# Performance work log

Measured on AMD Instinct MI355X. Metric: run time of the kernel, lower is better.

Reference implementation:

```python
import jax, jax.numpy as jnp
import numpy as np

B, QS, KS, E, H = 2, 2048, 2048, 2048, 16
D = E // H  # head_dim = 128
EPS = 1e-6


def setup_inputs() -> dict:
    key = jax.random.key(0)
    ks = jax.random.split(key, 11)
    scale_in = 1.0 / np.sqrt(E)  # lecun_normal fan_in = E
    scale_out = 1.0 / np.sqrt(E)  # fan_in for out proj = H*D = E
    return {
        "q": jax.random.normal(ks[0], (B, QS, E), jnp.float32),
        "kv": jax.random.normal(ks[1], (B, KS, E), jnp.float32),
        "q_pos": jax.random.normal(ks[2], (B, QS, E), jnp.float32),
        "kv_pos": jax.random.normal(ks[3], (B, KS, E), jnp.float32),
        "mask": jax.random.bernoulli(ks[4], 0.5, (B, QS, KS)),
        "wq": jax.random.normal(ks[5], (E, H, D), jnp.float32) * scale_in,
        "wk": jax.random.normal(ks[6], (E, H, D), jnp.float32) * scale_in,
        "wv": jax.random.normal(ks[7], (E, H, D), jnp.float32) * scale_in,
        "q_ln_scale": jnp.ones((D,), jnp.float32),
        "k_ln_scale": jnp.ones((D,), jnp.float32),
        "wo": jax.random.normal(ks[8], (H, D, E), jnp.float32) * scale_out,
    }


def _layernorm_no_bias(x, scale):
    # flax LayerNorm over last axis, use_bias=False, epsilon=1e-6
    mu = jnp.mean(x, axis=-1, keepdims=True)
    var = jnp.mean(jnp.square(x - mu), axis=-1, keepdims=True)
    return (x - mu) * jax.lax.rsqrt(var + EPS) * scale


def reference(q, kv, q_pos, kv_pos, mask, wq, wk, wv, q_ln_scale, k_ln_scale, wo):
    dtype = q.dtype
    qi = q + q_pos          # [b, qs, e]
    ki = kv + kv_pos        # [b, ks, e]
    vi = kv
    # QKV projections (DenseGeneral, no bias) -> [b, s, h, d]
    qh = jnp.einsum('bqe,ehd->bqhd', qi, wq)
    kh = jnp.einsum('bke,ehd->bkhd', ki, wk)
    vh = jnp.einsum('bke,ehd->bkhd', vi, wv)
    # normalize_qk: LayerNorm (no bias) on query/key over head_dim
    qh = _layernorm_no_bias(qh, q_ln_scale)
    kh = _layernorm_no_bias(kh, k_ln_scale)
    # scaled dot-product with float32 logits
    qh = qh / jnp.sqrt(jnp.asarray(D, dtype))
    logits = jnp.einsum('bqhd,bkhd->bhqk', qh, kh,
                        preferred_element_type=jnp.float32)
    big_neg = jnp.finfo(jnp.float32).min
    logits = jnp.where(mask[:, None, :, :], logits, big_neg)
    attn = jax.nn.softmax(logits, axis=-1).astype(dtype)  # [b,h,q,k]
    out = jnp.einsum('bhqk,bkhd->bqhd', attn, vh)
    # output projection (DenseGeneral over (h,d), no bias)
    return jnp.einsum('bqhd,hde->bqe', out, wo)
```

## Files before the change

### kernel.cpp

```cpp
#include <hip/hip_runtime.h>
#include <hip/hip_bf16.h>


typedef __attribute__((ext_vector_type(8))) __bf16 bf16x8;
typedef __attribute__((ext_vector_type(4))) float f32x4;
typedef __attribute__((ext_vector_type(8))) unsigned short ushort8;
typedef __attribute__((ext_vector_type(4))) unsigned short ushort4v;
typedef __attribute__((ext_vector_type(4))) unsigned uint4v;
typedef __attribute__((ext_vector_type(4))) float float4v;

#define MFMA16(a, b, c) __builtin_amdgcn_mfma_f32_16x16x32_bf16((a), (b), (c), 0, 0, 0)

__device__ __forceinline__ unsigned short f2bf(float f) {
  unsigned u = __builtin_bit_cast(unsigned, f);
  u += 0x7fffu + ((u >> 16) & 1u);
  return (unsigned short)(u >> 16);
}

__device__ __forceinline__ unsigned pkbf(float lo, float hi) {
  unsigned d;
  asm("v_cvt_pk_bf16_f32 %0, %1, %2" : "=v"(d) : "v"(lo), "v"(hi));
  return d;
}

__device__ __forceinline__ float max3f(float a, float b, float c) {
  float d;
  asm("v_max3_f32 %0, %1, %2, %3" : "=v"(d) : "v"(a), "v"(b), "v"(c));
  return d;
}

__device__ __forceinline__ float exp2a(float x) {
  float d;
  asm("v_exp_f32 %0, %1" : "=v"(d) : "v"(x));
  return d;
}

__device__ __forceinline__ void gload_lds16(const void* g, void* l) {
  __builtin_amdgcn_global_load_lds(
      (const __attribute__((address_space(1))) void*)g,
      (__attribute__((address_space(3))) void*)l, 16, 0, 0);
}

__global__ __launch_bounds__(256) void k_cvt(const float4v* __restrict__ x,
                                             const float4v* __restrict__ y,
                                             ushort4v* __restrict__ o, int n4) {
  int i = blockIdx.x * 256 + threadIdx.x;
  if (i >= n4) return;
  float4v a = x[i];
  if (y) { float4v b = y[i]; a = a + b; }
  ushort4v r;
  r[0] = f2bf(a[0]); r[1] = f2bf(a[1]); r[2] = f2bf(a[2]); r[3] = f2bf(a[3]);
  o[i] = r;
}

__global__ __launch_bounds__(256) void k_cvt2(const float4v* __restrict__ x,
                                              const float4v* __restrict__ y,
                                              ushort4v* __restrict__ oa,
                                              ushort4v* __restrict__ ob, int n4) {
  int i = blockIdx.x * 256 + threadIdx.x;
  if (i >= n4) return;
  float4v a = x[i];
  float4v s = a + y[i];
  ushort4v ra, rb;
  ra[0] = f2bf(s[0]); ra[1] = f2bf(s[1]); ra[2] = f2bf(s[2]); ra[3] = f2bf(s[3]);
  rb[0] = f2bf(a[0]); rb[1] = f2bf(a[1]); rb[2] = f2bf(a[2]); rb[3] = f2bf(a[3]);
  oa[i] = ra; ob[i] = rb;
}

__global__ __launch_bounds__(256) void k_tr(const float* __restrict__ s0, const float* __restrict__ s1,
                                            const float* __restrict__ s2, const float* __restrict__ s3,
                                            unsigned short* __restrict__ d0, unsigned short* __restrict__ d1,
                                            unsigned short* __restrict__ d2, unsigned short* __restrict__ d3) {
  __shared__ float t[32][33];
  const float* S; unsigned short* D;
  switch (blockIdx.z) {
    case 0: S = s0; D = d0; break;
    case 1: S = s1; D = d1; break;
    case 2: S = s2; D = d2; break;
    default: S = s3; D = d3; break;
  }
  int x = threadIdx.x & 31, y = threadIdx.x >> 5;
  int r0 = blockIdx.y * 32, c0 = blockIdx.x * 32;
#pragma unroll
  for (int i = 0; i < 4; ++i) t[y + 8 * i][x] = S[(size_t)(r0 + y + 8 * i) * 2048 + c0 + x];
  __syncthreads();
#pragma unroll
  for (int i = 0; i < 4; ++i)
    D[(size_t)(c0 + y + 8 * i) * 2048 + r0 + x] = f2bf(t[x][y + 8 * i]);
}

__global__ __launch_bounds__(256) void k_mask(const int* __restrict__ m,
                                              unsigned long long* __restrict__ out) {
  int i = blockIdx.x * 256 + threadIdx.x;
  unsigned long long b = __ballot(m[i] != 0);
  if ((threadIdx.x & 63) == 0) out[i >> 6] = b;
}

__global__ __launch_bounds__(256) void k_trv(const unsigned short* __restrict__ Vh,
                                             unsigned short* __restrict__ Vt) {
  __shared__ unsigned short t[64][72];
  int bh = blockIdx.z;
  int s0 = blockIdx.x * 64, d0 = blockIdx.y * 64;
  size_t base = (size_t)bh * 2048 * 128;
  int row = threadIdx.x >> 2, c16 = (threadIdx.x & 3) * 16;
  {
    const unsigned short* src = Vh + base + (size_t)(s0 + row) * 128 + d0 + c16;
    ushort8 a0 = *(const ushort8*)src;
    ushort8 a1 = *(const ushort8*)(src + 8);
#pragma unroll
    for (int e = 0; e < 8; ++e) {
      t[c16 + e][row] = a0[e];
      t[c16 + 8 + e][row] = a1[e];
    }
  }
  __syncthreads();
  {
    unsigned short* dst = Vt + base + (size_t)(d0 + row) * 2048 + s0 + c16;
    *(ushort8*)dst = *(const ushort8*)&t[row][c16];
    *(ushort8*)(dst + 8) = *(const ushort8*)&t[row][c16 + 8];
  }
}

template <int MODE>
__global__ __launch_bounds__(256) void k_gemm(const unsigned short* __restrict__ A,
                                              const unsigned short* __restrict__ Bt,
                                              void* __restrict__ Cv,
                                              const float* __restrict__ lnsc) {
  constexpr int K = 2048;
  __shared__ __attribute__((aligned(16))) unsigned short sA[128 * 64];
  __shared__ __attribute__((aligned(16))) unsigned short sB[128 * 64];
  __shared__ float sSum[2][128];
  __shared__ float sSq[2][128];
  int tid = threadIdx.x;
  int lane = tid & 63, w = tid >> 6;
  int wr = w >> 1, wc = w & 1;
  int r15 = lane & 15, blk = lane >> 4;
  int n0 = blockIdx.x * 128, m0 = blockIdx.y * 128;
  const unsigned short* Abase = A + (size_t)m0 * K;
  const unsigned short* Bbase = Bt + (size_t)n0 * K;
  f32x4 acc[4][4] = {};

  for (int kt = 0; kt < K; kt += 64) {
#pragma unroll
    for (int i = 0; i < 4; ++i) {
      int c = i * 256 + tid;
      int row = c >> 3, cc = c & 7;
      gload_lds16(Abase + (size_t)row * K + kt + ((cc ^ (row & 7)) * 8), &sA[c * 8]);
    }
#pragma unroll
    for (int i = 0; i < 4; ++i) {
      int c = i * 256 + tid;
      int row = c >> 3, cc = c & 7;
      gload_lds16(Bbase + (size_t)row * K + kt + ((cc ^ (row & 7)) * 8), &sB[c * 8]);
    }
    __syncthreads();
#pragma unroll
    for (int kk = 0; kk < 2; ++kk) {
      bf16x8 av[4], bv[4];
#pragma unroll
      for (int i = 0; i < 4; ++i) {
        int row = wr * 64 + i * 16 + r15;
        av[i] = *(const bf16x8*)&sA[row * 64 + (((kk * 4 + blk) ^ (row & 7)) * 8)];
      }
#pragma unroll
      for (int j = 0; j < 4; ++j) {
        int row = wc * 64 + j * 16 + r15;
        bv[j] = *(const bf16x8*)&sB[row * 64 + (((kk * 4 + blk) ^ (row & 7)) * 8)];
      }
#pragma unroll
      for (int i = 0; i < 4; ++i)
#pragma unroll
        for (int j = 0; j < 4; ++j) acc[i][j] = MFMA16(av[i], bv[j], acc[i][j]);
    }
    __syncthreads();
  }

  if constexpr (MODE == 3) {
    float* C = (float*)Cv;
#pragma unroll
    for (int i = 0; i < 4; ++i)
#pragma unroll
      for (int r = 0; r < 4; ++r)
#pragma unroll
        for (int j = 0; j < 4; ++j) {
          int rowl = wr * 64 + i * 16 + blk * 4 + r;
          int coll = wc * 64 + j * 16 + r15;
          C[(size_t)(m0 + rowl) * 2048 + n0 + coll] = acc[i][j][r];
        }
    return;
  } else {
    if constexpr (MODE == 1 || MODE == 2) {
#pragma unroll
      for (int i = 0; i < 4; ++i)
#pragma unroll
        for (int r = 0; r < 4; ++r) {
          float sm = 0.f, sq = 0.f;
#pragma unroll
          for (int j = 0; j < 4; ++j) { float v = acc[i][j][r]; sm += v; sq += v * v; }
          sm += __shfl_xor(sm, 1); sq += __shfl_xor(sq, 1);
          sm += __shfl_xor(sm, 2); sq += __shfl_xor(sq, 2);
          sm += __shfl_xor(sm, 4); sq += __shfl_xor(sq, 4);
          sm += __shfl_xor(sm, 8); sq += __shfl_xor(sq, 8);
          if (r15 == 0) {
            int rowl = wr * 64 + i * 16 + blk * 4 + r;
            sSum[wc][rowl] = sm; sSq[wc][rowl] = sq;
          }
        }
      __syncthreads();
    }
    unsigned short* Hout = (unsigned short*)Cv;
    int h = blockIdx.x;
#pragma unroll
    for (int i = 0; i < 4; ++i)
#pragma unroll
      for (int r = 0; r < 4; ++r) {
        int rowl = wr * 64 + i * 16 + blk * 4 + r;
        float mean = 0.f, rstd = 1.f;
        if constexpr (MODE == 1 || MODE == 2) {
          float sm = sSum[0][rowl] + sSum[1][rowl];
          float sq = sSq[0][rowl] + sSq[1][rowl];
          mean = sm * 0.0078125f;
          float var = sq * 0.0078125f - mean * mean;
          rstd = rsqrtf(var + 1e-6f);
        }
        int rowg = m0 + rowl;
        int b = rowg >> 11, s = rowg & 2047;
        unsigned short* orow = Hout + (((size_t)b * 16 + h) * 2048 + s) * 128;
#pragma unroll
        for (int j = 0; j < 4; ++j) {
          int d = wc * 64 + j * 16 + r15;
          float v = acc[i][j][r];
          if constexpr (MODE == 1)
            v = (v - mean) * rstd * lnsc[d] * (0.08838834764831845f * 1.4426950408889634f);
          if constexpr (MODE == 2) v = (v - mean) * rstd * lnsc[d];
          orow[d] = f2bf(v);
        }
      }
  }
}

__device__ __forceinline__ void softmax_grp(const f32x4 (&st)[4], unsigned mw0, unsigned mw1,
                                            int blk, float& mv, float& ls,
                                            f32x4 (&o)[8], bf16x8& plo, bf16x8& phi) {
  unsigned mws0 = mw0 >> (blk * 8);
  unsigned mws1 = mw1 >> (blk * 8);
  float pvv[16];
#pragma unroll
  for (int t = 0; t < 16; ++t) {
    int s = t >> 2, r = t & 3;
    unsigned mws = (s & 2) ? mws1 : mws0;
    int bit = 4 * (s & 1) + r;
    pvv[t] = ((mws >> bit) & 1u) ? st[s][r] : -1e30f;
  }
  float c0 = max3f(pvv[0], pvv[1], pvv[2]);
  float c1 = max3f(pvv[3], pvv[4], pvv[5]);
  float c2 = max3f(pvv[6], pvv[7], pvv[8]);
  float c3 = max3f(pvv[9], pvv[10], pvv[11]);
  float c4 = max3f(pvv[12], pvv[13], pvv[14]);
  float cmax = fmaxf(max3f(c0, c1, c2), max3f(c3, c4, pvv[15]));
  cmax = fmaxf(cmax, __shfl_xor(cmax, 16));
  cmax = fmaxf(cmax, __shfl_xor(cmax, 32));
  if (!__all(cmax - mv <= 11.5f)) {
    float mnew = fmaxf(mv, cmax);
    float fac = exp2a(mv - mnew);
    ls *= fac;
    float fr0 = __shfl(fac, blk * 4 + 0);
    float fr1 = __shfl(fac, blk * 4 + 1);
    float fr2 = __shfl(fac, blk * 4 + 2);
    float fr3 = __shfl(fac, blk * 4 + 3);
#pragma unroll
    for (int t8 = 0; t8 < 8; ++t8) {
      o[t8][0] *= fr0; o[t8][1] *= fr1; o[t8][2] *= fr2; o[t8][3] *= fr3;
    }
    mv = mnew;
  }
#pragma unroll
  for (int t = 0; t < 16; ++t) pvv[t] = exp2a(pvv[t] - mv);
  float s0 = (pvv[0] + pvv[1]) + (pvv[2] + pvv[3]);
  float s1 = (pvv[4] + pvv[5]) + (pvv[6] + pvv[7]);
  float s2 = (pvv[8] + pvv[9]) + (pvv[10] + pvv[11]);
  float s3 = (pvv[12] + pvv[13]) + (pvv[14] + pvv[15]);
  ls += (s0 + s1) + (s2 + s3);
  uint4v w0, w1;
#pragma unroll
  for (int j = 0; j < 4; ++j) {
    w0[j] = pkbf(pvv[2 * j], pvv[2 * j + 1]);
    w1[j] = pkbf(pvv[8 + 2 * j], pvv[9 + 2 * j]);
  }
  plo = __builtin_bit_cast(bf16x8, w0);
  phi = __builtin_bit_cast(bf16x8, w1);
}

__global__ __launch_bounds__(512, 4) void k_attn(const unsigned short* __restrict__ Qh,
                                                 const unsigned short* __restrict__ Kh,
                                                 const unsigned short* __restrict__ Vt,
                                                 const unsigned* __restrict__ maskb,
                                                 unsigned short* __restrict__ O) {
  __shared__ __attribute__((aligned(16))) char smem[65536];
  int tid = threadIdx.x, w = tid >> 6;
  int lane = tid & 63;
  int r15 = lane & 15, blk = lane >> 4;
  int bh = blockIdx.y, b = bh >> 4, h = bh & 15;
  int qb = blockIdx.x * 128;
  size_t base = (size_t)bh * (2048 * 128);
  int qrow = qb + w * 16 + r15;

  bf16x8 qf[4];
  {
    const unsigned short* qp = Qh + base + (size_t)qrow * 128 + blk * 8;
#pragma unroll
    for (int kk = 0; kk < 4; ++kk) qf[kk] = *(const bf16x8*)(qp + kk * 32);
  }
  const unsigned* mrow = maskb + ((size_t)b * 2048 + qrow) * 64;

  const unsigned short* kgp[2];
  const unsigned short* vgp[2];
#pragma unroll
  for (int i = 0; i < 2; ++i) {
    int c = i * 512 + tid;
    int rr = c >> 4, cc = c & 15;
    int key = 32 * (rr >> 5) + 8 * ((rr >> 2) & 3) + 4 * ((rr >> 4) & 1) + (rr & 3);
    kgp[i] = Kh + base + (size_t)key * 128 + ((cc ^ (rr & 7)) * 8);
    int d = c >> 3, c8 = c & 7;
    vgp[i] = Vt + base + (size_t)d * 2048 + ((c8 ^ (d & 7)) * 8);
  }

  f32x4 o[8] = {};
  float mv = -1e30f, ls = 0.f;

#pragma unroll
  for (int i = 0; i < 2; ++i) {
    int c = i * 512 + tid;
    gload_lds16(kgp[i], (unsigned short*)smem + c * 8);
    gload_lds16(vgp[i], (unsigned short*)(smem + 16384) + c * 8);
  }
  __syncthreads();

  int cur = 0;
  for (int kc = 0; kc < 2048; kc += 64) {
    if (kc + 64 < 2048) {
      char* nb = smem + ((cur ^ 1) << 15);
#pragma unroll
      for (int i = 0; i < 2; ++i) {
        int c = i * 512 + tid;
        gload_lds16(kgp[i] + (size_t)(kc + 64) * 128, (unsigned short*)nb + c * 8);
        gload_lds16(vgp[i] + (kc + 64), (unsigned short*)(nb + 16384) + c * 8);
      }
    }
    const unsigned short* sK = (const unsigned short*)(smem + (cur << 15));
    const unsigned short* sV = (const unsigned short*)(smem + (cur << 15) + 16384);

    f32x4 st[4] = {};
#pragma unroll
    for (int kk = 0; kk < 4; ++kk) {
      int cc = (4 * kk + blk) ^ (r15 & 7);
#pragma unroll
      for (int s = 0; s < 4; ++s) {
        bf16x8 kf = *(const bf16x8*)&sK[(16 * s + r15) * 128 + cc * 8];
        st[s] = MFMA16(kf, qf[kk], st[s]);
      }
    }

    unsigned mw0 = mrow[kc >> 5], mw1 = mrow[(kc >> 5) + 1];
    bf16x8 pf0, pf1;
    softmax_grp(st, mw0, mw1, blk, mv, ls, o, pf0, pf1);

#pragma unroll
    for (int t8 = 0; t8 < 8; ++t8) {
      int vr = t8 * 16 + r15;
      bf16x8 v0 = *(const bf16x8*)&sV[vr * 64 + ((blk ^ (r15 & 7)) * 8)];
      bf16x8 v1 = *(const bf16x8*)&sV[vr * 64 + (((4 + blk) ^ (r15 & 7)) * 8)];
      o[t8] = MFMA16(pf0, v0, o[t8]);
      o[t8] = MFMA16(pf1, v1, o[t8]);
    }
    __syncthreads();
    cur ^= 1;
  }

  ls += __shfl_xor(ls, 16);
  ls += __shfl_xor(ls, 32);
  float inv = 1.f / ls;
  float ir0 = __shfl(inv, blk * 4 + 0), ir1 = __shfl(inv, blk * 4 + 1);
  float ir2 = __shfl(inv, blk * 4 + 2), ir3 = __shfl(inv, blk * 4 + 3);

  float* sO = (float*)smem;
  __syncthreads();
#pragma unroll
  for (int pass = 0; pass < 2; ++pass) {
    if ((w >> 2) == pass) {
      int wl = w & 3;
#pragma unroll
      for (int t8 = 0; t8 < 8; ++t8) {
        int bi = (wl * 16 + blk * 4) * 132 + t8 * 16 + r15;
        sO[bi] = o[t8][0] * ir0;
        sO[bi + 132] = o[t8][1] * ir1;
        sO[bi + 264] = o[t8][2] * ir2;
        sO[bi + 396] = o[t8][3] * ir3;
      }
    }
    __syncthreads();
    {
      int row = tid >> 3, d0 = (tid & 7) * 16;
      int grow = qb + pass * 64 + row;
      unsigned short* op = O + (size_t)(b * 2048 + grow) * 2048 + h * 128 + d0;
      ushort8 pk0, pk1;
#pragma unroll
      for (int e = 0; e < 8; ++e) {
        pk0[e] = f2bf(sO[row * 132 + d0 + e]);
        pk1[e] = f2bf(sO[row * 132 + d0 + 8 + e]);
      }
      *(ushort8*)op = pk0;
      *(ushort8*)(op + 8) = pk1;
    }
    __syncthreads();
  }
}

extern "C" void kernel_launch(void* const* d_in, const int* in_sizes, int n_in,
                              void* d_out, int out_size, void* d_ws, size_t ws_size,
                              hipStream_t stream) {
  const float* q      = (const float*)d_in[0];
  const float* kv     = (const float*)d_in[1];
  const float* q_pos  = (const float*)d_in[2];
  const float* kv_pos = (const float*)d_in[3];
  const int*   mask   = (const int*)d_in[4];
  const float* wq     = (const float*)d_in[5];
  const float* wk     = (const float*)d_in[6];
  const float* wv     = (const float*)d_in[7];
  const float* qls    = (const float*)d_in[8];
  const float* kls    = (const float*)d_in[9];
  const float* wo     = (const float*)d_in[10];

  char* ws = (char*)d_ws;
  const size_t SZ_ACT = (size_t)4096 * 2048 * 2;
  const size_t SZ_W   = (size_t)2048 * 2048 * 2;
  unsigned short* a_q = (unsigned short*)(ws);
  unsigned short* a_k = (unsigned short*)(ws + SZ_ACT);
  unsigned short* a_v = (unsigned short*)(ws + 2 * SZ_ACT);
  unsigned short* Qh  = (unsigned short*)(ws + 3 * SZ_ACT);
  unsigned short* Kh  = (unsigned short*)(ws + 4 * SZ_ACT);
  unsigned short* Vh  = (unsigned short*)(ws + 5 * SZ_ACT);
  unsigned short* wqt = (unsigned short*)(ws + 6 * SZ_ACT);
  unsigned short* wkt = (unsigned short*)(ws + 6 * SZ_ACT + SZ_W);
  unsigned short* wvt = (unsigned short*)(ws + 6 * SZ_ACT + 2 * SZ_W);
  unsigned short* wot = (unsigned short*)(ws + 6 * SZ_ACT + 3 * SZ_W);
  unsigned*       mkb = (unsigned*)(ws + 6 * SZ_ACT + 4 * SZ_W);
  unsigned short* Ob  = a_q;
  unsigned short* Vtr = a_k;

  const size_t NEED = 6 * SZ_ACT + 4 * SZ_W + (size_t)2 * 2048 * 64 * 4;
  if (ws_size < NEED) return;

  k_cvt<<<8192, 256, 0, stream>>>((const float4v*)q, (const float4v*)q_pos, (ushort4v*)a_q, 2097152);
  k_cvt2<<<8192, 256, 0, stream>>>((const float4v*)kv, (const float4v*)kv_pos,
                                   (ushort4v*)a_k, (ushort4v*)a_v, 2097152);
  k_tr<<<dim3(64, 64, 4), 256, 0, stream>>>(wq, wk, wv, wo, wqt, wkt, wvt, wot);
  k_mask<<<32768, 256, 0, stream>>>(mask, (unsigned long long*)mkb);

  k_gemm<1><<<dim3(16, 32), 256, 0, stream>>>(a_q, wqt, Qh, qls);
  k_gemm<2><<<dim3(16, 32), 256, 0, stream>>>(a_k, wkt, Kh, kls);
  k_gemm<0><<<dim3(16, 32), 256, 0, stream>>>(a_v, wvt, Vh, nullptr);

  k_trv<<<dim3(32, 2, 32), 256, 0, stream>>>(Vh, Vtr);

  k_attn<<<dim3(16, 32), 512, 0, stream>>>(Qh, Kh, Vtr, mkb, Ob);

  k_gemm<3><<<dim3(16, 32), 256, 0, stream>>>(Ob, wot, d_out, nullptr);
}
```

Before: 353.3 us.

## Switch attention kernel to 32x32x16 MFMA with 4 waves per block

```diff
diff --git a/kernel.cpp b/kernel.cpp
--- a/kernel.cpp
+++ b/kernel.cpp
@@ -4,12 +4,14 @@
 
 typedef __attribute__((ext_vector_type(8))) __bf16 bf16x8;
 typedef __attribute__((ext_vector_type(4))) float f32x4;
+typedef __attribute__((ext_vector_type(16))) float f32x16;
 typedef __attribute__((ext_vector_type(8))) unsigned short ushort8;
 typedef __attribute__((ext_vector_type(4))) unsigned short ushort4v;
 typedef __attribute__((ext_vector_type(4))) unsigned uint4v;
 typedef __attribute__((ext_vector_type(4))) float float4v;
 
 #define MFMA16(a, b, c) __builtin_amdgcn_mfma_f32_16x16x32_bf16((a), (b), (c), 0, 0, 0)
+#define MFMA32(a, b, c) __builtin_amdgcn_mfma_f32_32x32x16_bf16((a), (b), (c), 0, 0, 0)
 
 __device__ __forceinline__ unsigned short f2bf(float f) {
   unsigned u = __builtin_bit_cast(unsigned, f);
@@ -115,9 +117,17 @@
   }
   __syncthreads();
   {
+    const int P0[8] = {0, 1, 2, 3, 8, 9, 10, 11};
+    const int P1[8] = {4, 5, 6, 7, 12, 13, 14, 15};
     unsigned short* dst = Vt + base + (size_t)(d0 + row) * 2048 + s0 + c16;
-    *(ushort8*)dst = *(const ushort8*)&t[row][c16];
-    *(ushort8*)(dst + 8) = *(const ushort8*)&t[row][c16 + 8];
+    ushort8 w0, w1;
+#pragma unroll
+    for (int e = 0; e < 8; ++e) {
+      w0[e] = t[row][c16 + P0[e]];
+      w1[e] = t[row][c16 + P1[e]];
+    }
+    *(ushort8*)dst = w0;
+    *(ushort8*)(dst + 8) = w1;
   }
 }
 
@@ -239,100 +249,47 @@
   }
 }
 
-__device__ __forceinline__ void softmax_grp(const f32x4 (&st)[4], unsigned mw0, unsigned mw1,
-                                            int blk, float& mv, float& ls,
-                                            f32x4 (&o)[8], bf16x8& plo, bf16x8& phi) {
-  unsigned mws0 = mw0 >> (blk * 8);
-  unsigned mws1 = mw1 >> (blk * 8);
-  float pvv[16];
-#pragma unroll
-  for (int t = 0; t < 16; ++t) {
-    int s = t >> 2, r = t & 3;
-    unsigned mws = (s & 2) ? mws1 : mws0;
-    int bit = 4 * (s & 1) + r;
-    pvv[t] = ((mws >> bit) & 1u) ? st[s][r] : -1e30f;
-  }
-  float c0 = max3f(pvv[0], pvv[1], pvv[2]);
-  float c1 = max3f(pvv[3], pvv[4], pvv[5]);
-  float c2 = max3f(pvv[6], pvv[7], pvv[8]);
-  float c3 = max3f(pvv[9], pvv[10], pvv[11]);
-  float c4 = max3f(pvv[12], pvv[13], pvv[14]);
-  float cmax = fmaxf(max3f(c0, c1, c2), max3f(c3, c4, pvv[15]));
-  cmax = fmaxf(cmax, __shfl_xor(cmax, 16));
-  cmax = fmaxf(cmax, __shfl_xor(cmax, 32));
-  if (!__all(cmax - mv <= 11.5f)) {
-    float mnew = fmaxf(mv, cmax);
-    float fac = exp2a(mv - mnew);
-    ls *= fac;
-    float fr0 = __shfl(fac, blk * 4 + 0);
-    float fr1 = __shfl(fac, blk * 4 + 1);
-    float fr2 = __shfl(fac, blk * 4 + 2);
-    float fr3 = __shfl(fac, blk * 4 + 3);
-#pragma unroll
-    for (int t8 = 0; t8 < 8; ++t8) {
-      o[t8][0] *= fr0; o[t8][1] *= fr1; o[t8][2] *= fr2; o[t8][3] *= fr3;
-    }
-    mv = mnew;
-  }
-#pragma unroll
-  for (int t = 0; t < 16; ++t) pvv[t] = exp2a(pvv[t] - mv);
-  float s0 = (pvv[0] + pvv[1]) + (pvv[2] + pvv[3]);
-  float s1 = (pvv[4] + pvv[5]) + (pvv[6] + pvv[7]);
-  float s2 = (pvv[8] + pvv[9]) + (pvv[10] + pvv[11]);
-  float s3 = (pvv[12] + pvv[13]) + (pvv[14] + pvv[15]);
-  ls += (s0 + s1) + (s2 + s3);
-  uint4v w0, w1;
-#pragma unroll
-  for (int j = 0; j < 4; ++j) {
-    w0[j] = pkbf(pvv[2 * j], pvv[2 * j + 1]);
-    w1[j] = pkbf(pvv[8 + 2 * j], pvv[9 + 2 * j]);
-  }
-  plo = __builtin_bit_cast(bf16x8, w0);
-  phi = __builtin_bit_cast(bf16x8, w1);
-}
-
-__global__ __launch_bounds__(512, 4) void k_attn(const unsigned short* __restrict__ Qh,
+__global__ __launch_bounds__(256, 2) void k_attn(const unsigned short* __restrict__ Qh,
                                                  const unsigned short* __restrict__ Kh,
-                                                 const unsigned short* __restrict__ Vt,
+                                                 const unsigned short* __restrict__ Vtp,
                                                  const unsigned* __restrict__ maskb,
                                                  unsigned short* __restrict__ O) {
   __shared__ __attribute__((aligned(16))) char smem[65536];
   int tid = threadIdx.x, w = tid >> 6;
   int lane = tid & 63;
-  int r15 = lane & 15, blk = lane >> 4;
+  int q31 = lane & 31, hi = lane >> 5;
   int bh = blockIdx.y, b = bh >> 4, h = bh & 15;
   int qb = blockIdx.x * 128;
   size_t base = (size_t)bh * (2048 * 128);
-  int qrow = qb + w * 16 + r15;
-
-  bf16x8 qf[4];
+  int qrow = qb + w * 32 + q31;
+
+  bf16x8 qf[8];
   {
-    const unsigned short* qp = Qh + base + (size_t)qrow * 128 + blk * 8;
-#pragma unroll
-    for (int kk = 0; kk < 4; ++kk) qf[kk] = *(const bf16x8*)(qp + kk * 32);
+    const unsigned short* qp = Qh + base + (size_t)qrow * 128 + hi * 8;
+#pragma unroll
+    for (int wd = 0; wd < 8; ++wd) qf[wd] = *(const bf16x8*)(qp + wd * 16);
   }
   const unsigned* mrow = maskb + ((size_t)b * 2048 + qrow) * 64;
 
-  const unsigned short* kgp[2];
-  const unsigned short* vgp[2];
-#pragma unroll
-  for (int i = 0; i < 2; ++i) {
-    int c = i * 512 + tid;
+  const unsigned short* kgp[4];
+  const unsigned short* vgp[4];
+#pragma unroll
+  for (int i = 0; i < 4; ++i) {
+    int c = i * 256 + tid;
     int rr = c >> 4, cc = c & 15;
-    int key = 32 * (rr >> 5) + 8 * ((rr >> 2) & 3) + 4 * ((rr >> 4) & 1) + (rr & 3);
-    kgp[i] = Kh + base + (size_t)key * 128 + ((cc ^ (rr & 7)) * 8);
+    kgp[i] = Kh + base + (size_t)rr * 128 + ((cc ^ (rr & 15)) * 8);
     int d = c >> 3, c8 = c & 7;
-    vgp[i] = Vt + base + (size_t)d * 2048 + ((c8 ^ (d & 7)) * 8);
-  }
-
-  f32x4 o[8] = {};
+    vgp[i] = Vtp + base + (size_t)d * 2048 + ((c8 ^ (d & 7)) * 8);
+  }
+
+  f32x16 o[4] = {};
   float mv = -1e30f, ls = 0.f;
 
 #pragma unroll
-  for (int i = 0; i < 2; ++i) {
-    int c = i * 512 + tid;
-    gload_lds16(kgp[i], (unsigned short*)smem + c * 8);
-    gload_lds16(vgp[i], (unsigned short*)(smem + 16384) + c * 8);
+  for (int i = 0; i < 4; ++i) {
+    int c = i * 256 + tid;
+    gload_lds16(kgp[i], smem + c * 16);
+    gload_lds16(vgp[i], smem + 16384 + c * 16);
   }
   __syncthreads();
 
@@ -341,78 +298,134 @@
     if (kc + 64 < 2048) {
       char* nb = smem + ((cur ^ 1) << 15);
 #pragma unroll
-      for (int i = 0; i < 2; ++i) {
-        int c = i * 512 + tid;
-        gload_lds16(kgp[i] + (size_t)(kc + 64) * 128, (unsigned short*)nb + c * 8);
-        gload_lds16(vgp[i] + (kc + 64), (unsigned short*)(nb + 16384) + c * 8);
+      for (int i = 0; i < 4; ++i) {
+        int c = i * 256 + tid;
+        gload_lds16(kgp[i] + (size_t)(kc + 64) * 128, nb + c * 16);
+        gload_lds16(vgp[i] + (kc + 64), nb + 16384 + c * 16);
       }
     }
     const unsigned short* sK = (const unsigned short*)(smem + (cur << 15));
     const unsigned short* sV = (const unsigned short*)(smem + (cur << 15) + 16384);
 
-    f32x4 st[4] = {};
-#pragma unroll
-    for (int kk = 0; kk < 4; ++kk) {
-      int cc = (4 * kk + blk) ^ (r15 & 7);
-#pragma unroll
-      for (int s = 0; s < 4; ++s) {
-        bf16x8 kf = *(const bf16x8*)&sK[(16 * s + r15) * 128 + cc * 8];
-        st[s] = MFMA16(kf, qf[kk], st[s]);
-      }
-    }
-
-    unsigned mw0 = mrow[kc >> 5], mw1 = mrow[(kc >> 5) + 1];
-    bf16x8 pf0, pf1;
-    softmax_grp(st, mw0, mw1, blk, mv, ls, o, pf0, pf1);
-
-#pragma unroll
-    for (int t8 = 0; t8 < 8; ++t8) {
-      int vr = t8 * 16 + r15;
-      bf16x8 v0 = *(const bf16x8*)&sV[vr * 64 + ((blk ^ (r15 & 7)) * 8)];
-      bf16x8 v1 = *(const bf16x8*)&sV[vr * 64 + (((4 + blk) ^ (r15 & 7)) * 8)];
-      o[t8] = MFMA16(pf0, v0, o[t8]);
-      o[t8] = MFMA16(pf1, v1, o[t8]);
+    unsigned mw0 = mrow[kc >> 5] >> (4 * hi);
+    unsigned mw1 = mrow[(kc >> 5) + 1] >> (4 * hi);
+
+    f32x16 st0 = {}, st1 = {};
+#pragma unroll
+    for (int wd = 0; wd < 8; ++wd) {
+      int ck = ((2 * wd + hi) ^ (q31 & 15)) * 8;
+      bf16x8 k0 = *(const bf16x8*)&sK[q31 * 128 + ck];
+      bf16x8 k1 = *(const bf16x8*)&sK[(32 + q31) * 128 + ck];
+      st0 = MFMA32(k0, qf[wd], st0);
+      st1 = MFMA32(k1, qf[wd], st1);
+    }
+
+    float pvv[32];
+#pragma unroll
+    for (int r = 0; r < 16; ++r) {
+      int bit = (r & 3) + 8 * (r >> 2);
+      pvv[r] = ((mw0 >> bit) & 1u) ? st0[r] : -1e30f;
+      pvv[16 + r] = ((mw1 >> bit) & 1u) ? st1[r] : -1e30f;
+    }
+    float c0 = max3f(pvv[0], pvv[1], pvv[2]);
+    float c1 = max3f(pvv[3], pvv[4], pvv[5]);
+    float c2 = max3f(pvv[6], pvv[7], pvv[8]);
+    float c3 = max3f(pvv[9], pvv[10], pvv[11]);
+    float c4 = max3f(pvv[12], pvv[13], pvv[14]);
+    float c5 = max3f(pvv[15], pvv[16], pvv[17]);
+    float c6 = max3f(pvv[18], pvv[19], pvv[20]);
+    float c7 = max3f(pvv[21], pvv[22], pvv[23]);
+    float c8 = max3f(pvv[24], pvv[25], pvv[26]);
+    float c9 = max3f(pvv[27], pvv[28], pvv[29]);
+    float ca = fmaxf(pvv[30], pvv[31]);
+    float t0 = max3f(c0, c1, c2);
+    float t1 = max3f(c3, c4, c5);
+    float t2 = max3f(c6, c7, c8);
+    float t3 = max3f(c9, ca, t0);
+    float cmax = max3f(t1, t2, t3);
+    cmax = fmaxf(cmax, __shfl_xor(cmax, 32));
+
+    if (!__all(cmax - mv <= 11.5f)) {
+      float mnew = fmaxf(mv, cmax);
+      float fac = exp2a(mv - mnew);
+      ls *= fac;
+      float fr[16];
+#pragma unroll
+      for (int r = 0; r < 16; ++r) fr[r] = __shfl(fac, (r & 3) + 8 * (r >> 2) + 4 * hi);
+#pragma unroll
+      for (int dt = 0; dt < 4; ++dt)
+#pragma unroll
+        for (int r = 0; r < 16; ++r) o[dt][r] *= fr[r];
+      mv = mnew;
+    }
+
+#pragma unroll
+    for (int t = 0; t < 32; ++t) pvv[t] = exp2a(pvv[t] - mv);
+    {
+      float s0 = 0.f, s1 = 0.f, s2 = 0.f, s3 = 0.f;
+#pragma unroll
+      for (int t = 0; t < 8; ++t) {
+        s0 += pvv[t]; s1 += pvv[8 + t]; s2 += pvv[16 + t]; s3 += pvv[24 + t];
+      }
+      ls += (s0 + s1) + (s2 + s3);
+    }
+
+    bf16x8 pa[4];
+#pragma unroll
+    for (int kw = 0; kw < 4; ++kw) {
+      uint4v pw;
+#pragma unroll
+      for (int m = 0; m < 4; ++m) pw[m] = pkbf(pvv[8 * kw + 2 * m], pvv[8 * kw + 2 * m + 1]);
+      pa[kw] = __builtin_bit_cast(bf16x8, pw);
+    }
+
+#pragma unroll
+    for (int dt = 0; dt < 4; ++dt) {
+      int vrow = dt * 32 + q31;
+#pragma unroll
+      for (int kw = 0; kw < 4; ++kw) {
+        int cv = ((2 * kw + hi) ^ (q31 & 7)) * 8;
+        bf16x8 vf = *(const bf16x8*)&sV[vrow * 64 + cv];
+        o[dt] = MFMA32(pa[kw], vf, o[dt]);
+      }
     }
     __syncthreads();
     cur ^= 1;
   }
 
-  ls += __shfl_xor(ls, 16);
   ls += __shfl_xor(ls, 32);
   float inv = 1.f / ls;
-  float ir0 = __shfl(inv, blk * 4 + 0), ir1 = __shfl(inv, blk * 4 + 1);
-  float ir2 = __shfl(inv, blk * 4 + 2), ir3 = __shfl(inv, blk * 4 + 3);
+  float ir[16];
+#pragma unroll
+  for (int r = 0; r < 16; ++r) ir[r] = __shfl(inv, (r & 3) + 8 * (r >> 2) + 4 * hi);
 
   float* sO = (float*)smem;
-  __syncthreads();
 #pragma unroll
   for (int pass = 0; pass < 2; ++pass) {
-    if ((w >> 2) == pass) {
-      int wl = w & 3;
-#pragma unroll
-      for (int t8 = 0; t8 < 8; ++t8) {
-        int bi = (wl * 16 + blk * 4) * 132 + t8 * 16 + r15;
-        sO[bi] = o[t8][0] * ir0;
-        sO[bi + 132] = o[t8][1] * ir1;
-        sO[bi + 264] = o[t8][2] * ir2;
-        sO[bi + 396] = o[t8][3] * ir3;
-      }
+    __syncthreads();
+    if ((w >> 1) == pass) {
+      int wl = w & 1;
+#pragma unroll
+      for (int dt = 0; dt < 4; ++dt)
+#pragma unroll
+        for (int r = 0; r < 16; ++r) {
+          int qrl = wl * 32 + (r & 3) + 8 * (r >> 2) + 4 * hi;
+          sO[qrl * 132 + dt * 32 + q31] = o[dt][r] * ir[r];
+        }
     }
     __syncthreads();
     {
-      int row = tid >> 3, d0 = (tid & 7) * 16;
+      int row = tid >> 2, d0 = (tid & 3) * 32;
       int grow = qb + pass * 64 + row;
       unsigned short* op = O + (size_t)(b * 2048 + grow) * 2048 + h * 128 + d0;
-      ushort8 pk0, pk1;
-#pragma unroll
-      for (int e = 0; e < 8; ++e) {
-        pk0[e] = f2bf(sO[row * 132 + d0 + e]);
-        pk1[e] = f2bf(sO[row * 132 + d0 + 8 + e]);
-      }
-      *(ushort8*)op = pk0;
-      *(ushort8*)(op + 8) = pk1;
-    }
-    __syncthreads();
+#pragma unroll
+      for (int g = 0; g < 4; ++g) {
+        ushort8 pk;
+#pragma unroll
+        for (int e = 0; e < 8; ++e) pk[e] = f2bf(sO[row * 132 + d0 + g * 8 + e]);
+        *(ushort8*)(op + g * 8) = pk;
+      }
+    }
   }
 }
 
@@ -463,7 +476,7 @@
 
   k_trv<<<dim3(32, 2, 32), 256, 0, stream>>>(Vh, Vtr);
 
-  k_attn<<<dim3(16, 32), 512, 0, stream>>>(Qh, Kh, Vtr, mkb, Ob);
+  k_attn<<<dim3(16, 32), 256, 0, stream>>>(Qh, Kh, Vtr, mkb, Ob);
 
   k_gemm<3><<<dim3(16, 32), 256, 0, stream>>>(Ob, wot, d_out, nullptr);
 }
```

Result: no change. 350.7 us (-0.7%).
